# Kernel tuning notes

Hardware: AMD Instinct MI355X
Metric: run time of the kernel (lower is better)

Reference implementation:

```python
import jax, jax.numpy as jnp
import numpy as np

T, D = 2048, 2048
N = 16
DN, DR, DV = 128, 64, 128   # qk_nope_head_dim, qk_rope_head_dim, v_head_dim
RQ, RKV = 1536, 512         # q_lora_rank, kv_lora_rank
EPS = 1e-6
THETA = 10000.0


def rmsnorm(x, scale, eps=EPS):
    var = jnp.mean(jnp.square(x), axis=-1, keepdims=True)
    return x * jax.lax.rsqrt(var + eps) * scale


def apply_rope(x, pos, theta=THETA):
    # x: [T, dr] or [T, N, dr]; rotate-half (NeoX) rotary embedding
    dr = x.shape[-1]
    half = dr // 2
    inv_freq = theta ** (-jnp.arange(half, dtype=jnp.float32) / half)
    freqs = pos.astype(jnp.float32)[:, None] * inv_freq  # [T, half]
    cos, sin = jnp.cos(freqs), jnp.sin(freqs)
    while cos.ndim < x.ndim:
        cos, sin = cos[:, None, :], sin[:, None, :]
    x1, x2 = jnp.split(x, 2, axis=-1)
    return jnp.concatenate([x1 * cos - x2 * sin, x2 * cos + x1 * sin], axis=-1).astype(x.dtype)


def setup_inputs() -> dict:
    key = jax.random.key(0)
    ks = jax.random.split(key, 6)
    s = 0.02
    return {
        'x': jax.random.normal(ks[0], (T, D), jnp.float32),
        'positions': jnp.arange(T, dtype=jnp.int32),
        'w_q_a': jax.random.normal(ks[1], (D, RQ), jnp.float32) * s,
        'q_a_norm': jnp.ones((RQ,), jnp.float32),
        'w_q_b': jax.random.normal(ks[2], (RQ, N * (DN + DR)), jnp.float32) * s,
        'w_kv_a': jax.random.normal(ks[3], (D, RKV + DR), jnp.float32) * s,
        'kv_a_norm': jnp.ones((RKV,), jnp.float32),
        'w_kv_b': jax.random.normal(ks[4], (RKV, N * (DN + DV)), jnp.float32) * s,
        'w_o': jax.random.normal(ks[5], (N * DV, D), jnp.float32) * s,
    }


def reference(x, positions, w_q_a, q_a_norm, w_q_b, w_kv_a, kv_a_norm, w_kv_b, w_o):
    t = x.shape[0]
    # --- low-rank Q projection ---
    q_c = rmsnorm(x @ w_q_a, q_a_norm)                      # [T, RQ]
    q = (q_c @ w_q_b).reshape(t, N, DN + DR)                # [T, N, DN+DR]
    q_nope, q_pe = q[..., :DN], q[..., DN:]
    q_pe = apply_rope(q_pe, positions)                      # [T, N, DR]
    # --- low-rank KV projection with shared rope key (MQA-style k_pe) ---
    kv = x @ w_kv_a                                          # [T, RKV+DR]
    kv_c, k_pe = kv[:, :RKV], kv[:, RKV:]
    kv_c = rmsnorm(kv_c, kv_a_norm)                          # [T, RKV]
    k_pe = apply_rope(k_pe, positions)                       # [T, DR]
    kvb = (kv_c @ w_kv_b).reshape(t, N, DN + DV)             # [T, N, DN+DV]
    k_nope, v = kvb[..., :DN], kvb[..., DN:]
    # --- causal attention, scale over full qk head dim ---
    scale = (DN + DR) ** -0.5
    scores = (jnp.einsum('tnh,snh->nts', q_nope, k_nope)
              + jnp.einsum('tnh,sh->nts', q_pe, k_pe)) * scale   # [N, T, T]
    causal = positions[:, None] >= positions[None, :]
    scores = jnp.where(causal[None, :, :], scores, jnp.finfo(scores.dtype).min)
    p = jax.nn.softmax(scores, axis=-1)
    out = jnp.einsum('nts,snv->tnv', p, v).reshape(t, N * DV)
    return out @ w_o                                          # [T, D]
```

## Files before the change

### kernel.cpp

```cpp
#include <hip/hip_runtime.h>
#include <hip/hip_bf16.h>
#include <math.h>

#define T_TOK   2048
#define NHEADS  16
#define EPS_    1e-6f
#define THETA_  10000.0f

typedef __attribute__((ext_vector_type(8))) short short8v;
typedef __attribute__((ext_vector_type(4))) float f32x4;

__device__ inline unsigned short f2bf(float f) {
    union { float f; unsigned u; } v; v.f = f;
    unsigned r = v.u + 0x7fffu + ((v.u >> 16) & 1u);
    return (unsigned short)(r >> 16);
}
__device__ inline float bf2f(unsigned short b) {
    return __uint_as_float(((unsigned)b) << 16);
}

__device__ __forceinline__ void gload16(const unsigned short* src, unsigned short* lds) {
    __builtin_amdgcn_global_load_lds(
        (const __attribute__((address_space(1))) unsigned int*)src,
        (__attribute__((address_space(3))) unsigned int*)lds, 16, 0, 0);
}

__device__ inline float block_reduce(float v, bool is_max, float* sred) {
    #pragma unroll
    for (int off = 32; off > 0; off >>= 1) {
        float o = __shfl_down(v, off, 64);
        v = is_max ? fmaxf(v, o) : (v + o);
    }
    int tid = threadIdx.x;
    __syncthreads();
    if ((tid & 63) == 0) sred[tid >> 6] = v;
    __syncthreads();
    float r = sred[0];
    #pragma unroll
    for (int w = 1; w < 4; ++w) r = is_max ? fmaxf(r, sred[w]) : (r + sred[w]);
    return r;
}

__global__ __launch_bounds__(256) void conv_bf16(const float* __restrict__ in,
    unsigned short* __restrict__ out, int n4)
{
    int i = blockIdx.x * 256 + threadIdx.x;
    if (i >= n4) return;
    float4 v = ((const float4*)in)[i];
    ushort4 o;
    o.x = f2bf(v.x); o.y = f2bf(v.y); o.z = f2bf(v.z); o.w = f2bf(v.w);
    ((ushort4*)out)[i] = o;
}

__global__ __launch_bounds__(256) void wt_bf16(const float* __restrict__ W,
    unsigned short* __restrict__ Wt, int R, int C)
{
    __shared__ float tile[32][33];
    int c0 = blockIdx.x * 32, r0 = blockIdx.y * 32;
    int tx = threadIdx.x & 31, ty = threadIdx.x >> 5;
    #pragma unroll
    for (int i = 0; i < 4; ++i)
        tile[ty + i * 8][tx] = W[(size_t)(r0 + ty + i * 8) * C + c0 + tx];
    __syncthreads();
    #pragma unroll
    for (int i = 0; i < 4; ++i)
        Wt[(size_t)(c0 + ty + i * 8) * R + r0 + tx] = f2bf(tile[tx][ty + i * 8]);
}

#define STAGE_GEMM(buf, k0)                                                   \
    {   _Pragma("unroll")                                                     \
        for (int p = 0; p < 4; ++p) {                                         \
            int u = p * 256 + tid;                                            \
            int r = u >> 3, cu = u & 7;                                       \
            int dst = (p * 256 + wid * 64) * 8;                               \
            gload16(A  + (size_t)(r0 + r) * K + (k0) + ((cu ^ (r & 7)) << 3), \
                    As[buf] + dst);                                           \
            gload16(Bt + (size_t)(c0 + r) * K + (k0) + ((cu ^ (r & 7)) << 3), \
                    Bs[buf] + dst);                                           \
        }                                                                     \
    }

#define GEMM_BODY()                                                           \
    STAGE_GEMM(0, 0)                                                          \
    const int nkt = K >> 6;                                                   \
    int buf = 0;                                                              \
    for (int kt = 0; kt < nkt; ++kt) {                                        \
        if (kt + 1 < nkt) {                                                   \
            STAGE_GEMM(buf ^ 1, (kt + 1) << 6)                                \
            asm volatile("s_waitcnt vmcnt(8)" ::: "memory");                  \
        } else {                                                              \
            asm volatile("s_waitcnt vmcnt(0)" ::: "memory");                  \
        }                                                                     \
        __builtin_amdgcn_s_barrier();                                         \
        _Pragma("unroll")                                                     \
        for (int ks = 0; ks < 2; ++ks) {                                      \
            short8v af[4], bf[4];                                             \
            _Pragma("unroll")                                                 \
            for (int m = 0; m < 4; ++m) {                                     \
                int row = wr * 64 + m * 16 + lrow;                            \
                af[m] = *(const short8v*)((char*)As[buf] + row * 128 +        \
                        (((ks * 4 + lkg) ^ (row & 7)) << 4));                 \
            }                                                                 \
            _Pragma("unroll")                                                 \
            for (int n = 0; n < 4; ++n) {                                     \
                int row = wc * 64 + n * 16 + lrow;                            \
                bf[n] = *(const short8v*)((char*)Bs[buf] + row * 128 +        \
                        (((ks * 4 + lkg) ^ (row & 7)) << 4));                 \
            }                                                                 \
            _Pragma("unroll")                                                 \
            for (int m = 0; m < 4; ++m)                                       \
                _Pragma("unroll")                                             \
                for (int n = 0; n < 4; ++n)                                   \
                    acc[m][n] = __builtin_amdgcn_mfma_f32_16x16x32_bf16(      \
                        af[m], bf[n], acc[m][n], 0, 0, 0);                    \
        }                                                                     \
        __builtin_amdgcn_s_barrier();                                         \
        buf ^= 1;                                                             \
    }

template<bool BF16OUT>
__global__ __launch_bounds__(256) void gemm_bf16(
    const unsigned short* __restrict__ A,
    const unsigned short* __restrict__ Bt,
    void* __restrict__ Cv, int N, int K, int ldc, float oscale)
{
    __shared__ __align__(16) unsigned short As[2][128 * 64];
    __shared__ __align__(16) unsigned short Bs[2][128 * 64];
    const int tid = threadIdx.x;
    const int lane = tid & 63, wid = tid >> 6;
    const int wr = wid >> 1, wc = wid & 1;
    const int lrow = lane & 15, lkg = lane >> 4;
    const int r0 = blockIdx.y * 128, c0 = blockIdx.x * 128;

    f32x4 acc[4][4];
    #pragma unroll
    for (int m = 0; m < 4; ++m)
        #pragma unroll
        for (int n = 0; n < 4; ++n) acc[m][n] = (f32x4)0.f;

    GEMM_BODY()

    #pragma unroll
    for (int m = 0; m < 4; ++m) {
        int grow = r0 + wr * 64 + m * 16 + lkg * 4;
        #pragma unroll
        for (int n = 0; n < 4; ++n) {
            int gcol = c0 + wc * 64 + n * 16 + lrow;
            if (gcol < N) {
                #pragma unroll
                for (int j = 0; j < 4; ++j) {
                    float v = acc[m][n][j] * oscale;
                    if (BF16OUT)
                        ((unsigned short*)Cv)[(size_t)(grow + j) * ldc + gcol] = f2bf(v);
                    else
                        ((float*)Cv)[(size_t)(grow + j) * ldc + gcol] = v;
                }
            }
        }
    }
}

__global__ __launch_bounds__(256) void gemm_kv(
    const unsigned short* __restrict__ A,
    const unsigned short* __restrict__ Bt,
    unsigned short* __restrict__ Kc,
    unsigned short* __restrict__ Vtc)
{
    __shared__ __align__(16) unsigned short As[2][128 * 64];
    __shared__ __align__(16) unsigned short Bs[2][128 * 64];
    const int tid = threadIdx.x;
    const int lane = tid & 63, wid = tid >> 6;
    const int wr = wid >> 1, wc = wid & 1;
    const int lrow = lane & 15, lkg = lane >> 4;
    const int r0 = blockIdx.y * 128, c0 = blockIdx.x * 128;
    const int K = 512;

    f32x4 acc[4][4];
    #pragma unroll
    for (int m = 0; m < 4; ++m)
        #pragma unroll
        for (int n = 0; n < 4; ++n) acc[m][n] = (f32x4)0.f;

    GEMM_BODY()

    #pragma unroll
    for (int m = 0; m < 4; ++m) {
        int grow = r0 + wr * 64 + m * 16 + lkg * 4;
        #pragma unroll
        for (int n = 0; n < 4; ++n) {
            int gcol = c0 + wc * 64 + n * 16 + lrow;
            int head = gcol >> 8, c = gcol & 255;
            if (c < 128) {
                #pragma unroll
                for (int j = 0; j < 4; ++j)
                    Kc[((size_t)head * 2048 + grow + j) * 192 + c] = f2bf(acc[m][n][j]);
            } else {
                ushort4 o;
                o.x = f2bf(acc[m][n][0]); o.y = f2bf(acc[m][n][1]);
                o.z = f2bf(acc[m][n][2]); o.w = f2bf(acc[m][n][3]);
                *(ushort4*)(Vtc + ((size_t)head * 128 + (c - 128)) * 2048 + grow) = o;
            }
        }
    }
}

__global__ __launch_bounds__(256) void rms_kv(const float* __restrict__ qkv,
    const float* __restrict__ gq, const float* __restrict__ gkv,
    const int* __restrict__ positions, unsigned short* __restrict__ q_cb,
    unsigned short* __restrict__ kv_cb, float* __restrict__ kpe)
{
    __shared__ float sred[4];
    int row = blockIdx.x, tid = threadIdx.x;
    const float* p = qkv + (size_t)row * 2112;

    float ss = 0.f;
    for (int i = tid; i < 1536; i += 256) { float v = p[i]; ss += v * v; }
    ss = block_reduce(ss, false, sred);
    float sc = rsqrtf(ss / 1536.0f + EPS_);
    for (int i = tid; i < 1536; i += 256)
        q_cb[(size_t)row * 1536 + i] = f2bf(p[i] * sc * gq[i]);

    float s2 = 0.f;
    for (int i = tid; i < 512; i += 256) { float v = p[1536 + i]; s2 += v * v; }
    s2 = block_reduce(s2, false, sred);
    float sc2 = rsqrtf(s2 / 512.0f + EPS_);
    for (int i = tid; i < 512; i += 256)
        kv_cb[(size_t)row * 512 + i] = f2bf(p[1536 + i] * sc2 * gkv[i]);

    if (tid < 32) {
        int i = tid;
        float pos = (float)positions[row];
        float inv = powf(THETA_, -(float)i / 32.0f);
        float ang = pos * inv;
        float c = cosf(ang), s = sinf(ang);
        float x1 = p[2048 + i], x2 = p[2080 + i];
        kpe[(size_t)row * 64 + i]      = x1 * c - x2 * s;
        kpe[(size_t)row * 64 + 32 + i] = x2 * c + x1 * s;
    }
}

__global__ __launch_bounds__(256) void kpe_kc(const float* __restrict__ kpe,
    unsigned short* __restrict__ Kc)
{
    int t = blockIdx.x, tid = threadIdx.x;
    int n = tid >> 4, i4 = (tid & 15) * 4;
    float4 p = *(const float4*)(kpe + (size_t)t * 64 + i4);
    ushort4 o; o.x = f2bf(p.x); o.y = f2bf(p.y); o.z = f2bf(p.z); o.w = f2bf(p.w);
    *(ushort4*)(Kc + ((size_t)n * 2048 + t) * 192 + 128 + i4) = o;
}

__global__ __launch_bounds__(256) void rope_fix(unsigned short* __restrict__ qb,
    const int* __restrict__ positions)
{
    int t = blockIdx.x, tid = threadIdx.x;
    int n = tid >> 4;
    int i0 = (tid & 15) * 2;
    float pos = (float)positions[t];
    unsigned short* p = qb + ((size_t)t * 16 + n) * 192 + 128;
    #pragma unroll
    for (int e = 0; e < 2; ++e) {
        int i = i0 + e;
        float inv = powf(THETA_, -(float)i / 32.0f);
        float ang = pos * inv;
        float c = cosf(ang), s = sinf(ang);
        float x1 = bf2f(p[i]), x2 = bf2f(p[32 + i]);
        p[i]      = f2bf(x1 * c - x2 * s);
        p[32 + i] = f2bf(x2 * c + x1 * s);
    }
}

#define QBLK  64
#define KVBLK 64
#define NCH   3

__global__ __launch_bounds__(256) void attn_part(
    const unsigned short* __restrict__ qb,
    const unsigned short* __restrict__ Kc,
    const unsigned short* __restrict__ Vtc,
    unsigned short* __restrict__ Opart,
    float2* __restrict__ Ml)
{
    __shared__ __align__(16) unsigned short Ks[KVBLK * 192];
    __shared__ __align__(16) unsigned short Vt[128 * KVBLK];
    __shared__ __align__(16) unsigned short Ps[4][16 * KVBLK];

    const int bid = blockIdx.x;
    const int xcd = bid & 7;
    const int j   = bid >> 3;
    const int n   = xcd * 2 + (j >= 96);
    const int jj  = (j >= 96) ? j - 96 : j;
    const int qt  = 31 - (jj / NCH);
    const int ch  = jj % NCH;

    const int nt  = qt + 1;
    const int csz = (nt + NCH - 1) / NCH;
    const int tstart = ch * csz;
    if (tstart >= nt) return;
    const int tend = min(tstart + csz, nt);

    const int tid = threadIdx.x;
    const int lane = tid & 63, wid = tid >> 6;
    const int lrow = lane & 15;
    const int lkg  = lane >> 4;
    const int q0 = qt * QBLK;
    const int qrow_g = q0 + wid * 16 + lrow;
    const int pidx = ((n * 32 + qt) * NCH + ch);

    const unsigned short* Kh = Kc  + (size_t)n * 2048 * 192;
    const unsigned short* Vh = Vtc + (size_t)n * 128 * 2048;

    int koff[6], voff[4];
    #pragma unroll
    for (int p = 0; p < 6; ++p) {
        int u = p * 256 + tid;
        int row = u / 24, c8 = u % 24;
        koff[p] = row * 192 + ((c8 ^ (row & 7)) << 3);
    }
    #pragma unroll
    for (int p = 0; p < 4; ++p) {
        int u = p * 256 + tid;
        int dv = u >> 3, c8 = u & 7;
        voff[p] = dv * 2048 + ((c8 ^ (dv & 7)) << 3);
    }

    short8v qf[6];
    {
        const unsigned short* qrow = qb + ((size_t)qrow_g * 16 + n) * 192;
        #pragma unroll
        for (int ds = 0; ds < 6; ++ds)
            qf[ds] = *(const short8v*)(qrow + ds * 32 + lkg * 8);
    }

    f32x4 oacc[8];
    #pragma unroll
    for (int i = 0; i < 8; ++i) oacc[i] = (f32x4)0.f;
    float mrow = -3e38f;
    float lsum = 0.f;

    #pragma unroll
    for (int p = 0; p < 6; ++p)
        gload16(Kh + (size_t)tstart * KVBLK * 192 + koff[p], Ks + (p * 256 + wid * 64) * 8);
    #pragma unroll
    for (int p = 0; p < 4; ++p)
        gload16(Vh + tstart * KVBLK + voff[p], Vt + (p * 256 + wid * 64) * 8);

    for (int tile = tstart; tile < tend; ++tile) {
        const int s0 = tile * KVBLK;
        const bool more = (tile + 1 < tend);

        asm volatile("s_waitcnt vmcnt(4)" ::: "memory");
        __builtin_amdgcn_s_barrier();

        f32x4 sacc[4];
        #pragma unroll
        for (int ct = 0; ct < 4; ++ct) sacc[ct] = (f32x4)0.f;
        __builtin_amdgcn_s_setprio(1);
        #pragma unroll
        for (int ds = 0; ds < 6; ++ds) {
            #pragma unroll
            for (int ct = 0; ct < 4; ++ct) {
                int krow = ct * 16 + lrow;
                int byte = (krow * 384 + ds * 64 + lkg * 16) ^ ((krow & 7) << 4);
                short8v kf = *(const short8v*)((char*)Ks + byte);
                sacc[ct] = __builtin_amdgcn_mfma_f32_16x16x32_bf16(kf, qf[ds], sacc[ct], 0, 0, 0);
            }
        }
        __builtin_amdgcn_s_setprio(0);

        #pragma unroll
        for (int ct = 0; ct < 4; ++ct) {
            #pragma unroll
            for (int jq = 0; jq < 4; ++jq) {
                int key = s0 + ct * 16 + lkg * 4 + jq;
                if (key > qrow_g) sacc[ct][jq] = -3e38f;
            }
        }

        float tm = -3e38f;
        #pragma unroll
        for (int ct = 0; ct < 4; ++ct) {
            float a = fmaxf(sacc[ct][0], sacc[ct][1]);
            float b = fmaxf(sacc[ct][2], sacc[ct][3]);
            tm = fmaxf(tm, fmaxf(a, b));
        }
        tm = fmaxf(tm, __shfl_xor(tm, 16, 64));
        tm = fmaxf(tm, __shfl_xor(tm, 32, 64));

        const bool grow = !__all(tm <= mrow);
        float corr = 1.f;
        if (grow) {
            float mn = fmaxf(mrow, tm);
            corr = exp2f(mrow - mn);
            mrow = mn;
        }

        float psum = 0.f;
        unsigned short pb[4][4];
        #pragma unroll
        for (int ct = 0; ct < 4; ++ct)
            #pragma unroll
            for (int jq = 0; jq < 4; ++jq) {
                float sv = sacc[ct][jq];
                float p = (sv > -1e37f) ? exp2f(sv - mrow) : 0.f;
                psum += p;
                pb[ct][jq] = f2bf(p);
            }
        psum += __shfl_xor(psum, 16, 64);
        psum += __shfl_xor(psum, 32, 64);
        lsum = grow ? (lsum * corr + psum) : (lsum + psum);

        if (grow) {
            float corr4[4];
            #pragma unroll
            for (int jq = 0; jq < 4; ++jq)
                corr4[jq] = __shfl(corr, (lane & 48) | (lkg * 4 + jq), 64);
            #pragma unroll
            for (int dt = 0; dt < 8; ++dt)
                #pragma unroll
                for (int jq = 0; jq < 4; ++jq) oacc[dt][jq] *= corr4[jq];
        }

        #pragma unroll
        for (int ct = 0; ct < 4; ++ct) {
            int c0k = ct * 16 + lkg * 4;
            int byte = ((lrow * 64 + c0k) * 2) ^ ((lrow & 7) << 4);
            uint2 w;
            w.x = (unsigned)pb[ct][0] | ((unsigned)pb[ct][1] << 16);
            w.y = (unsigned)pb[ct][2] | ((unsigned)pb[ct][3] << 16);
            *(uint2*)((char*)Ps[wid] + byte) = w;
        }

        asm volatile("s_waitcnt vmcnt(0)" ::: "memory");
        __builtin_amdgcn_s_barrier();

        __builtin_amdgcn_s_setprio(1);
        #pragma unroll
        for (int ks = 0; ks < 2; ++ks) {
            int abyte = ((lrow * 64 + ks * 32 + lkg * 8) * 2) ^ ((lrow & 7) << 4);
            short8v af = *(const short8v*)((char*)Ps[wid] + abyte);
            #pragma unroll
            for (int dt = 0; dt < 8; ++dt) {
                int vrow = dt * 16 + lrow;
                int byte = ((vrow * 128 + ks * 64 + lkg * 16)) ^ ((vrow & 7) << 4);
                short8v bf = *(const short8v*)((char*)Vt + byte);
                oacc[dt] = __builtin_amdgcn_mfma_f32_16x16x32_bf16(af, bf, oacc[dt], 0, 0, 0);
            }
        }
        __builtin_amdgcn_s_setprio(0);

        __builtin_amdgcn_s_barrier();
        if (more) {
            const int s1 = s0 + KVBLK;
            #pragma unroll
            for (int p = 0; p < 6; ++p)
                gload16(Kh + (size_t)s1 * 192 + koff[p], Ks + (p * 256 + wid * 64) * 8);
            #pragma unroll
            for (int p = 0; p < 4; ++p)
                gload16(Vh + s1 + voff[p], Vt + (p * 256 + wid * 64) * 8);
        }
    }

    #pragma unroll
    for (int dt = 0; dt < 8; ++dt)
        #pragma unroll
        for (int jq = 0; jq < 4; ++jq) {
            int row = wid * 16 + lkg * 4 + jq;
            Opart[(size_t)pidx * 8192 + row * 128 + dt * 16 + lrow] = f2bf(oacc[dt][jq]);
        }
    if (lkg == 0)
        Ml[(size_t)pidx * 64 + wid * 16 + lrow] = make_float2(mrow, lsum);
}

__global__ __launch_bounds__(256) void attn_combine(
    const unsigned short* __restrict__ Opart, const float2* __restrict__ Ml,
    unsigned short* __restrict__ aob)
{
    const int bid = blockIdx.x;
    const int head = bid >> 5, qt = bid & 31;
    const int nt = qt + 1, csz = (nt + NCH - 1) / NCH;
    const int nch = (nt + csz - 1) / csz;
    const int tid = threadIdx.x;
    const int r = tid >> 2, qc = tid & 3;
    const int base = (head * 32 + qt) * NCH;

    float mi[NCH], li[NCH];
    float m = -3e38f;
    #pragma unroll
    for (int i = 0; i < NCH; ++i) {
        mi[i] = -3e38f; li[i] = 0.f;
        if (i < nch) {
            float2 v = Ml[(size_t)(base + i) * 64 + r];
            mi[i] = v.x; li[i] = v.y;
            m = fmaxf(m, v.x);
        }
    }
    float acc[32];
    #pragma unroll
    for (int u = 0; u < 32; ++u) acc[u] = 0.f;
    float l = 0.f;
    #pragma unroll
    for (int i = 0; i < NCH; ++i) {
        if (i < nch) {
            float w = exp2f(mi[i] - m);
            l += w * li[i];
            const unsigned short* op = Opart + (size_t)(base + i) * 8192 + r * 128 + qc * 32;
            #pragma unroll
            for (int u = 0; u < 4; ++u) {
                short8v v8 = *(const short8v*)(op + u * 8);
                #pragma unroll
                for (int e = 0; e < 8; ++e)
                    acc[u * 8 + e] += w * bf2f((unsigned short)v8[e]);
            }
        }
    }
    float invl = 1.0f / l;
    unsigned short* dst = aob + (size_t)(qt * 64 + r) * 2048 + head * 128 + qc * 32;
    #pragma unroll
    for (int u = 0; u < 4; ++u) {
        short8v o8;
        #pragma unroll
        for (int e = 0; e < 8; ++e) o8[e] = (short)f2bf(acc[u * 8 + e] * invl);
        *(short8v*)(dst + u * 8) = o8;
    }
}

extern "C" void kernel_launch(void* const* d_in, const int* in_sizes, int n_in,
                              void* d_out, int out_size, void* d_ws, size_t ws_size,
                              hipStream_t stream)
{
    const float* x         = (const float*)d_in[0];
    const int*   positions = (const int*)  d_in[1];
    const float* w_q_a     = (const float*)d_in[2];
    const float* q_a_norm  = (const float*)d_in[3];
    const float* w_q_b     = (const float*)d_in[4];
    const float* w_kv_a    = (const float*)d_in[5];
    const float* kv_a_norm = (const float*)d_in[6];
    const float* w_kv_b    = (const float*)d_in[7];
    const float* w_o       = (const float*)d_in[8];
    float* out = (float*)d_out;

    const float QSCALE = 0.07216878364870323f * 1.4426950408889634f;

    char* base = (char*)d_ws;
    unsigned short* Kc  = (unsigned short*)base;
    unsigned short* Vtc = Kc + (size_t)16 * 2048 * 192;
    char* pR1 = base + (size_t)2048 * 3072 * 4;
    float* qkv_c = (float*)pR1;
    unsigned short* Opart = (unsigned short*)pR1;
    float2* Ml = (float2*)(pR1 + (size_t)1536 * 8192 * 2);
    char* pR2 = pR1 + (size_t)1536 * 8192 * 2 + (size_t)1536 * 64 * 8;
    unsigned short* q_cb  = (unsigned short*)pR2;
    unsigned short* kv_cb = q_cb + (size_t)2048 * 1536;
    float* kpe = (float*)(kv_cb + (size_t)2048 * 512);
    char* pR3 = pR2 + (size_t)2048 * 1536 * 2 + (size_t)2048 * 512 * 2 + (size_t)2048 * 64 * 4;
    unsigned short* xb  = (unsigned short*)pR3;
    unsigned short* aob = xb;
    char* pR4 = pR3 + (size_t)2048 * 2048 * 2;
    unsigned short* qb = (unsigned short*)pR4;
    char* pR5 = pR4 + (size_t)2048 * 3072 * 2;
    unsigned short* wbuf = (unsigned short*)pR5;

    dim3 blk(256);

    conv_bf16<<<(2048 * 2048 / 4 + 255) / 256, blk, 0, stream>>>(x, xb, 2048 * 2048 / 4);

    wt_bf16<<<dim3(1536 / 32, 2048 / 32), blk, 0, stream>>>(w_q_a, wbuf, 2048, 1536);
    wt_bf16<<<dim3(576 / 32, 2048 / 32), blk, 0, stream>>>(w_kv_a, wbuf + (size_t)1536 * 2048, 2048, 576);
    gemm_bf16<false><<<dim3(17, 16), blk, 0, stream>>>(xb, wbuf, qkv_c, 2112, 2048, 2112, 1.0f);
    rms_kv<<<2048, blk, 0, stream>>>(qkv_c, q_a_norm, kv_a_norm, positions, q_cb, kv_cb, kpe);

    wt_bf16<<<dim3(3072 / 32, 1536 / 32), blk, 0, stream>>>(w_q_b, wbuf, 1536, 3072);
    gemm_bf16<true><<<dim3(3072 / 128, 16), blk, 0, stream>>>(q_cb, wbuf, qb, 3072, 1536, 3072, QSCALE);
    rope_fix<<<2048, blk, 0, stream>>>(qb, positions);

    kpe_kc<<<2048, blk, 0, stream>>>(kpe, Kc);

    wt_bf16<<<dim3(4096 / 32, 512 / 32), blk, 0, stream>>>(w_kv_b, wbuf, 512, 4096);
    gemm_kv<<<dim3(4096 / 128, 16), blk, 0, stream>>>(kv_cb, wbuf, Kc, Vtc);

    attn_part<<<1536, blk, 0, stream>>>(qb, Kc, Vtc, Opart, Ml);
    attn_combine<<<512, blk, 0, stream>>>(Opart, Ml, aob);

    wt_bf16<<<dim3(2048 / 32, 2048 / 32), blk, 0, stream>>>(w_o, wbuf, 2048, 2048);
    gemm_bf16<false><<<dim3(2048 / 128, 16), blk, 0, stream>>>(aob, wbuf, out, 2048, 2048, 2048, 1.0f);
}
```

Measured before the change: 225.1 us.

## Process two query tiles per attention block to share K/V tile loads

```diff
diff --git a/kernel.cpp b/kernel.cpp
--- a/kernel.cpp
+++ b/kernel.cpp
@@ -269,7 +269,6 @@
     }
 }
 
-#define QBLK  64
 #define KVBLK 64
 #define NCH   3
 
@@ -287,12 +286,12 @@
     const int bid = blockIdx.x;
     const int xcd = bid & 7;
     const int j   = bid >> 3;
-    const int n   = xcd * 2 + (j >= 96);
-    const int jj  = (j >= 96) ? j - 96 : j;
-    const int qt  = 31 - (jj / NCH);
+    const int n   = xcd * 2 + (j >= 48);
+    const int jj  = (j >= 48) ? j - 48 : j;
+    const int Q   = 15 - (jj / NCH);
     const int ch  = jj % NCH;
 
-    const int nt  = qt + 1;
+    const int nt  = 2 * Q + 2;
     const int csz = (nt + NCH - 1) / NCH;
     const int tstart = ch * csz;
     if (tstart >= nt) return;
@@ -302,9 +301,6 @@
     const int lane = tid & 63, wid = tid >> 6;
     const int lrow = lane & 15;
     const int lkg  = lane >> 4;
-    const int q0 = qt * QBLK;
-    const int qrow_g = q0 + wid * 16 + lrow;
-    const int pidx = ((n * 32 + qt) * NCH + ch);
 
     const unsigned short* Kh = Kc  + (size_t)n * 2048 * 192;
     const unsigned short* Vh = Vtc + (size_t)n * 128 * 2048;
@@ -323,19 +319,21 @@
         voff[p] = dv * 2048 + ((c8 ^ (dv & 7)) << 3);
     }
 
-    short8v qf[6];
-    {
-        const unsigned short* qrow = qb + ((size_t)qrow_g * 16 + n) * 192;
+    int qrow_g[2];
+    short8v qf[2][6];
+    f32x4 oacc[2][8];
+    float mrow[2] = {-3e38f, -3e38f};
+    float lsum[2] = {0.f, 0.f};
+    #pragma unroll
+    for (int s = 0; s < 2; ++s) {
+        qrow_g[s] = Q * 128 + s * 64 + wid * 16 + lrow;
+        const unsigned short* qrow = qb + ((size_t)qrow_g[s] * 16 + n) * 192;
         #pragma unroll
         for (int ds = 0; ds < 6; ++ds)
-            qf[ds] = *(const short8v*)(qrow + ds * 32 + lkg * 8);
-    }
-
-    f32x4 oacc[8];
-    #pragma unroll
-    for (int i = 0; i < 8; ++i) oacc[i] = (f32x4)0.f;
-    float mrow = -3e38f;
-    float lsum = 0.f;
+            qf[s][ds] = *(const short8v*)(qrow + ds * 32 + lkg * 8);
+        #pragma unroll
+        for (int i = 0; i < 8; ++i) oacc[s][i] = (f32x4)0.f;
+    }
 
     #pragma unroll
     for (int p = 0; p < 6; ++p)
@@ -351,102 +349,107 @@
         asm volatile("s_waitcnt vmcnt(4)" ::: "memory");
         __builtin_amdgcn_s_barrier();
 
-        f32x4 sacc[4];
-        #pragma unroll
-        for (int ct = 0; ct < 4; ++ct) sacc[ct] = (f32x4)0.f;
-        __builtin_amdgcn_s_setprio(1);
-        #pragma unroll
-        for (int ds = 0; ds < 6; ++ds) {
+        #pragma unroll
+        for (int s = 0; s < 2; ++s) {
+            f32x4 sacc[4];
+            #pragma unroll
+            for (int ct = 0; ct < 4; ++ct) sacc[ct] = (f32x4)0.f;
+            __builtin_amdgcn_s_setprio(1);
+            #pragma unroll
+            for (int ds = 0; ds < 6; ++ds) {
+                #pragma unroll
+                for (int ct = 0; ct < 4; ++ct) {
+                    int krow = ct * 16 + lrow;
+                    int byte = (krow * 384 + ds * 64 + lkg * 16) ^ ((krow & 7) << 4);
+                    short8v kf = *(const short8v*)((char*)Ks + byte);
+                    sacc[ct] = __builtin_amdgcn_mfma_f32_16x16x32_bf16(kf, qf[s][ds], sacc[ct], 0, 0, 0);
+                }
+            }
+            __builtin_amdgcn_s_setprio(0);
+
             #pragma unroll
             for (int ct = 0; ct < 4; ++ct) {
-                int krow = ct * 16 + lrow;
-                int byte = (krow * 384 + ds * 64 + lkg * 16) ^ ((krow & 7) << 4);
-                short8v kf = *(const short8v*)((char*)Ks + byte);
-                sacc[ct] = __builtin_amdgcn_mfma_f32_16x16x32_bf16(kf, qf[ds], sacc[ct], 0, 0, 0);
-            }
+                #pragma unroll
+                for (int jq = 0; jq < 4; ++jq) {
+                    int key = s0 + ct * 16 + lkg * 4 + jq;
+                    if (key > qrow_g[s]) sacc[ct][jq] = -3e38f;
+                }
+            }
+
+            float tm = -3e38f;
+            #pragma unroll
+            for (int ct = 0; ct < 4; ++ct) {
+                float a = fmaxf(sacc[ct][0], sacc[ct][1]);
+                float b = fmaxf(sacc[ct][2], sacc[ct][3]);
+                tm = fmaxf(tm, fmaxf(a, b));
+            }
+            tm = fmaxf(tm, __shfl_xor(tm, 16, 64));
+            tm = fmaxf(tm, __shfl_xor(tm, 32, 64));
+
+            const bool grow = !__all(tm <= mrow[s]);
+            float corr = 1.f;
+            if (grow) {
+                float mn = fmaxf(mrow[s], tm);
+                corr = exp2f(mrow[s] - mn);
+                mrow[s] = mn;
+            }
+
+            float psum = 0.f;
+            unsigned short pb[4][4];
+            #pragma unroll
+            for (int ct = 0; ct < 4; ++ct)
+                #pragma unroll
+                for (int jq = 0; jq < 4; ++jq) {
+                    float sv = sacc[ct][jq];
+                    float p = (sv > -1e37f) ? exp2f(sv - mrow[s]) : 0.f;
+                    psum += p;
+                    pb[ct][jq] = f2bf(p);
+                }
+            psum += __shfl_xor(psum, 16, 64);
+            psum += __shfl_xor(psum, 32, 64);
+            lsum[s] = grow ? (lsum[s] * corr + psum) : (lsum[s] + psum);
+
+            if (grow) {
+                float corr4[4];
+                #pragma unroll
+                for (int jq = 0; jq < 4; ++jq)
+                    corr4[jq] = __shfl(corr, (lane & 48) | (lkg * 4 + jq), 64);
+                #pragma unroll
+                for (int dt = 0; dt < 8; ++dt)
+                    #pragma unroll
+                    for (int jq = 0; jq < 4; ++jq) oacc[s][dt][jq] *= corr4[jq];
+            }
+
+            #pragma unroll
+            for (int ct = 0; ct < 4; ++ct) {
+                int c0k = ct * 16 + lkg * 4;
+                int byte = ((lrow * 64 + c0k) * 2) ^ ((lrow & 7) << 4);
+                uint2 w;
+                w.x = (unsigned)pb[ct][0] | ((unsigned)pb[ct][1] << 16);
+                w.y = (unsigned)pb[ct][2] | ((unsigned)pb[ct][3] << 16);
+                *(uint2*)((char*)Ps[wid] + byte) = w;
+            }
+
+            if (s == 0) {
+                asm volatile("s_waitcnt vmcnt(0)" ::: "memory");
+                __builtin_amdgcn_s_barrier();
+            }
+
+            __builtin_amdgcn_s_setprio(1);
+            #pragma unroll
+            for (int ks = 0; ks < 2; ++ks) {
+                int abyte = ((lrow * 64 + ks * 32 + lkg * 8) * 2) ^ ((lrow & 7) << 4);
+                short8v af = *(const short8v*)((char*)Ps[wid] + abyte);
+                #pragma unroll
+                for (int dt = 0; dt < 8; ++dt) {
+                    int vrow = dt * 16 + lrow;
+                    int byte = ((vrow * 128 + ks * 64 + lkg * 16)) ^ ((vrow & 7) << 4);
+                    short8v bf = *(const short8v*)((char*)Vt + byte);
+                    oacc[s][dt] = __builtin_amdgcn_mfma_f32_16x16x32_bf16(af, bf, oacc[s][dt], 0, 0, 0);
+                }
+            }
+            __builtin_amdgcn_s_setprio(0);
         }
-        __builtin_amdgcn_s_setprio(0);
-
-        #pragma unroll
-        for (int ct = 0; ct < 4; ++ct) {
-            #pragma unroll
-            for (int jq = 0; jq < 4; ++jq) {
-                int key = s0 + ct * 16 + lkg * 4 + jq;
-                if (key > qrow_g) sacc[ct][jq] = -3e38f;
-            }
-        }
-
-        float tm = -3e38f;
-        #pragma unroll
-        for (int ct = 0; ct < 4; ++ct) {
-            float a = fmaxf(sacc[ct][0], sacc[ct][1]);
-            float b = fmaxf(sacc[ct][2], sacc[ct][3]);
-            tm = fmaxf(tm, fmaxf(a, b));
-        }
-        tm = fmaxf(tm, __shfl_xor(tm, 16, 64));
-        tm = fmaxf(tm, __shfl_xor(tm, 32, 64));
-
-        const bool grow = !__all(tm <= mrow);
-        float corr = 1.f;
-        if (grow) {
-            float mn = fmaxf(mrow, tm);
-            corr = exp2f(mrow - mn);
-            mrow = mn;
-        }
-
-        float psum = 0.f;
-        unsigned short pb[4][4];
-        #pragma unroll
-        for (int ct = 0; ct < 4; ++ct)
-            #pragma unroll
-            for (int jq = 0; jq < 4; ++jq) {
-                float sv = sacc[ct][jq];
-                float p = (sv > -1e37f) ? exp2f(sv - mrow) : 0.f;
-                psum += p;
-                pb[ct][jq] = f2bf(p);
-            }
-        psum += __shfl_xor(psum, 16, 64);
-        psum += __shfl_xor(psum, 32, 64);
-        lsum = grow ? (lsum * corr + psum) : (lsum + psum);
-
-        if (grow) {
-            float corr4[4];
-            #pragma unroll
-            for (int jq = 0; jq < 4; ++jq)
-                corr4[jq] = __shfl(corr, (lane & 48) | (lkg * 4 + jq), 64);
-            #pragma unroll
-            for (int dt = 0; dt < 8; ++dt)
-                #pragma unroll
-                for (int jq = 0; jq < 4; ++jq) oacc[dt][jq] *= corr4[jq];
-        }
-
-        #pragma unroll
-        for (int ct = 0; ct < 4; ++ct) {
-            int c0k = ct * 16 + lkg * 4;
-            int byte = ((lrow * 64 + c0k) * 2) ^ ((lrow & 7) << 4);
-            uint2 w;
-            w.x = (unsigned)pb[ct][0] | ((unsigned)pb[ct][1] << 16);
-            w.y = (unsigned)pb[ct][2] | ((unsigned)pb[ct][3] << 16);
-            *(uint2*)((char*)Ps[wid] + byte) = w;
-        }
-
-        asm volatile("s_waitcnt vmcnt(0)" ::: "memory");
-        __builtin_amdgcn_s_barrier();
-
-        __builtin_amdgcn_s_setprio(1);
-        #pragma unroll
-        for (int ks = 0; ks < 2; ++ks) {
-            int abyte = ((lrow * 64 + ks * 32 + lkg * 8) * 2) ^ ((lrow & 7) << 4);
-            short8v af = *(const short8v*)((char*)Ps[wid] + abyte);
-            #pragma unroll
-            for (int dt = 0; dt < 8; ++dt) {
-                int vrow = dt * 16 + lrow;
-                int byte = ((vrow * 128 + ks * 64 + lkg * 16)) ^ ((vrow & 7) << 4);
-                short8v bf = *(const short8v*)((char*)Vt + byte);
-                oacc[dt] = __builtin_amdgcn_mfma_f32_16x16x32_bf16(af, bf, oacc[dt], 0, 0, 0);
-            }
-        }
-        __builtin_amdgcn_s_setprio(0);
 
         __builtin_amdgcn_s_barrier();
         if (more) {
@@ -461,14 +464,18 @@
     }
 
     #pragma unroll
-    for (int dt = 0; dt < 8; ++dt)
-        #pragma unroll
-        for (int jq = 0; jq < 4; ++jq) {
-            int row = wid * 16 + lkg * 4 + jq;
-            Opart[(size_t)pidx * 8192 + row * 128 + dt * 16 + lrow] = f2bf(oacc[dt][jq]);
-        }
-    if (lkg == 0)
-        Ml[(size_t)pidx * 64 + wid * 16 + lrow] = make_float2(mrow, lsum);
+    for (int s = 0; s < 2; ++s) {
+        const int pidx = ((n * 32 + 2 * Q + s) * NCH + ch);
+        #pragma unroll
+        for (int dt = 0; dt < 8; ++dt)
+            #pragma unroll
+            for (int jq = 0; jq < 4; ++jq) {
+                int row = wid * 16 + lkg * 4 + jq;
+                Opart[(size_t)pidx * 8192 + row * 128 + dt * 16 + lrow] = f2bf(oacc[s][dt][jq]);
+            }
+        if (lkg == 0)
+            Ml[(size_t)pidx * 64 + wid * 16 + lrow] = make_float2(mrow[s], lsum[s]);
+    }
 }
 
 __global__ __launch_bounds__(256) void attn_combine(
@@ -477,7 +484,8 @@
 {
     const int bid = blockIdx.x;
     const int head = bid >> 5, qt = bid & 31;
-    const int nt = qt + 1, csz = (nt + NCH - 1) / NCH;
+    const int nt = (qt | 1) + 1;
+    const int csz = (nt + NCH - 1) / NCH;
     const int nch = (nt + csz - 1) / csz;
     const int tid = threadIdx.x;
     const int r = tid >> 2, qc = tid & 3;
@@ -578,7 +586,7 @@
     wt_bf16<<<dim3(4096 / 32, 512 / 32), blk, 0, stream>>>(w_kv_b, wbuf, 512, 4096);
     gemm_kv<<<dim3(4096 / 128, 16), blk, 0, stream>>>(kv_cb, wbuf, Kc, Vtc);
 
-    attn_part<<<1536, blk, 0, stream>>>(qb, Kc, Vtc, Opart, Ml);
+    attn_part<<<768, blk, 0, stream>>>(qb, Kc, Vtc, Opart, Ml);
     attn_combine<<<512, blk, 0, stream>>>(Opart, Ml, aob);
 
     wt_bf16<<<dim3(2048 / 32, 2048 / 32), blk, 0, stream>>>(w_o, wbuf, 2048, 2048);
```

Result: slower. 255.5 us (+13.5%).
